# Kernel tuning notes

Measured on AMD Instinct MI355X. Metric: run time of the kernel, lower is better.

The kernel has to match this reference:

```python
import jax, jax.numpy as jnp
import numpy as np

B, S, D = 2, 2048, 2048
H, DK, DV, L = 16, 128, 128, 64


def setup_inputs() -> dict:
    key = jax.random.key(0)
    ks = jax.random.split(key, 16)
    sc = lambda fan_in: 1.0 / np.sqrt(fan_in)
    inp = {
        "queries": jax.random.normal(ks[0], (B, S, D), jnp.float32),
        "keys": jax.random.normal(ks[1], (B, S, D), jnp.float32),
        "values": jax.random.normal(ks[2], (B, S, D), jnp.float32),
        # weights stored [in, out]
        "Wq": jax.random.normal(ks[3], (D, DK * H), jnp.float32) * sc(D),
        "bq": jnp.zeros((DK * H,), jnp.float32),
        "Wlk": jax.random.normal(ks[4], (D, L * H), jnp.float32) * sc(D),
        "blk": jnp.zeros((L * H,), jnp.float32),
        "Wlv": jax.random.normal(ks[5], (D, L * H), jnp.float32) * sc(D),
        "blv": jnp.zeros((L * H,), jnp.float32),
        "Wkr": jax.random.normal(ks[6], (L, DK), jnp.float32) * sc(L),
        "bkr": jnp.zeros((DK,), jnp.float32),
        "Wvr": jax.random.normal(ks[7], (L, DV), jnp.float32) * sc(L),
        "bvr": jnp.zeros((DV,), jnp.float32),
        "Wo": jax.random.normal(ks[8], (DV * H, D), jnp.float32) * sc(DV * H),
        "bo": jnp.zeros((D,), jnp.float32),
    }
    return inp


def reference(queries, keys, values, Wq, bq, Wlk, blk, Wlv, blv, Wkr, bkr, Wvr, bvr, Wo, bo):
    b, sq, _ = queries.shape
    sk = keys.shape[1]
    # query projection -> [b, h, sq, dk]
    q = (queries @ Wq + bq).reshape(b, sq, H, DK).transpose(0, 2, 1, 3)
    # low-rank latent KV -> [b, sk, h, L]
    lat_k = (keys @ Wlk + blk).reshape(b, sk, H, L)
    lat_v = (values @ Wlv + blv).reshape(b, sk, H, L)
    # reconstruction -> [b, h, sk, dk/dv]
    k = (lat_k @ Wkr + bkr).transpose(0, 2, 1, 3)
    v = (lat_v @ Wvr + bvr).transpose(0, 2, 1, 3)
    scores = jnp.einsum("bhqd,bhkd->bhqk", q, k) / np.sqrt(DK).astype(np.float32)
    causal = jnp.triu(jnp.ones((sq, sk), dtype=bool), k=1)
    scores = jnp.where(causal, -jnp.inf, scores)
    attn = jax.nn.softmax(scores, axis=-1)
    out = jnp.einsum("bhqk,bhkd->bhqd", attn, v)
    out = out.transpose(0, 2, 1, 3).reshape(b, sq, H * DV)
    return out @ Wo + bo
```

## Files before the change

### kernel.cpp

```cpp
#include <hip/hip_runtime.h>
#include <hip/hip_bf16.h>

#define B_SZ    2
#define S_LEN   2048
#define D_MODEL 2048
#define N_HEADS 16
#define D_HEAD  128
#define L_RANK  64
#define M_ROWS  (B_SZ * S_LEN)
#define KD      2048
#define NT      (KD / 32)
#define NTK     (KD / 64)

typedef short          bf16x8 __attribute__((ext_vector_type(8)));
typedef float          f32x4  __attribute__((ext_vector_type(4)));
typedef float          f32x16 __attribute__((ext_vector_type(16)));
typedef unsigned short us4v   __attribute__((ext_vector_type(4)));
typedef unsigned short us8v   __attribute__((ext_vector_type(8)));
typedef unsigned int   u32x4  __attribute__((ext_vector_type(4)));

#define SCALE_Q 0.127517432f

static __device__ __forceinline__ unsigned short f2bf(float f) {
    unsigned int u = __float_as_uint(f);
    u += 0x7FFFu + ((u >> 16) & 1u);
    return (unsigned short)(u >> 16);
}

static __device__ __forceinline__ void gload16(const void* g, void* l) {
    __builtin_amdgcn_global_load_lds(
        (const __attribute__((address_space(1))) unsigned int*)g,
        (__attribute__((address_space(3))) unsigned int*)l, 16, 0, 0);
}

static __device__ __forceinline__ bf16x8 ds_read128(const unsigned short* p) {
    bf16x8 r;
    unsigned int a = (unsigned int)(size_t)
        (const __attribute__((address_space(3))) unsigned short*)p;
    asm volatile("ds_read_b128 %0, %1" : "=&v"(r) : "v"(a));
    return r;
}

static __device__ __forceinline__ float exp2_hw(float x) {
    float r; asm("v_exp_f32 %0, %1" : "=v"(r) : "v"(x)); return r;
}
static __device__ __forceinline__ unsigned int cvtpk_bf16(float a, float b) {
    unsigned int r; asm("v_cvt_pk_bf16_f32 %0, %1, %2" : "=v"(r) : "v"(a), "v"(b)); return r;
}

__global__ __launch_bounds__(256) void prep_kernel(
    const float* __restrict__ q_in, const float* __restrict__ k_in,
    const float* __restrict__ v_in,
    const float* __restrict__ Wq, const float* __restrict__ Wlk,
    const float* __restrict__ Wlv, const float* __restrict__ Wo,
    const float* __restrict__ Wkr, const float* __restrict__ Wvr,
    unsigned short* __restrict__ q_o, unsigned short* __restrict__ k_o,
    unsigned short* __restrict__ v_o,
    unsigned short* __restrict__ WqT, unsigned short* __restrict__ WlkT,
    unsigned short* __restrict__ WlvT, unsigned short* __restrict__ WoT,
    unsigned short* __restrict__ WkrT, unsigned short* __restrict__ WvrT)
{
    __shared__ float tl[64][69];
    const int bid = blockIdx.x, tid = threadIdx.x;

    if (bid < 12288) {
        const int z = bid >> 12;
        const float* in = z == 0 ? q_in : (z == 1 ? k_in : v_in);
        unsigned short* out = z == 0 ? q_o : (z == 1 ? k_o : v_o);
        size_t i = ((size_t)(bid & 4095) * 256 + tid) * 8;
        float4 a = *(const float4*)&in[i];
        float4 b = *(const float4*)&in[i + 4];
        us8v o = { f2bf(a.x), f2bf(a.y), f2bf(a.z), f2bf(a.w),
                   f2bf(b.x), f2bf(b.y), f2bf(b.z), f2bf(b.w) };
        *(us8v*)&out[i] = o;
    } else if (bid < 16384) {
        const int t = bid - 12288;
        const int z = t >> 10;
        const int y = (t & 1023) >> 5, x = t & 31;
        const int Nz = (z == 1 || z == 2) ? 1024 : 2048;
        if (x * 64 >= Nz) return;
        const float* W = z == 0 ? Wq : (z == 1 ? Wlk : (z == 2 ? Wlv : Wo));
        unsigned short* WT = z == 0 ? WqT : (z == 1 ? WlkT : (z == 2 ? WlvT : WoT));
        const int k0 = y * 64, n0 = x * 64;
        #pragma unroll
        for (int c = 0; c < 4; ++c) {
            int idx = c * 256 + tid;
            int r = idx >> 4, c4 = (idx & 15) * 4;
            float4 v = *(const float4*)&W[(size_t)(k0 + r) * Nz + n0 + c4];
            tl[r][c4] = v.x; tl[r][c4 + 1] = v.y; tl[r][c4 + 2] = v.z; tl[r][c4 + 3] = v.w;
        }
        __syncthreads();
        #pragma unroll
        for (int c = 0; c < 2; ++c) {
            int idx = c * 256 + tid;
            int nr = idx >> 3, s = idx & 7;
            us8v o;
            #pragma unroll
            for (int j = 0; j < 8; ++j) o[j] = f2bf(tl[s * 8 + j][nr]);
            *(us8v*)&WT[(size_t)(n0 + nr) * KD + k0 + s * 8] = o;
        }
    } else {
        #pragma unroll 1
        for (int t2 = 0; t2 < 2; ++t2) {
            const float* W = t2 ? Wvr : Wkr;
            unsigned short* WT = t2 ? WvrT : WkrT;
            for (int i = 0; i < 32; ++i) {
                int e = i * 256 + tid;
                int d = e >> 6, l = e & 63;
                WT[d * 64 + l] = f2bf(W[l * 128 + d]);
            }
        }
    }
}

__global__ __launch_bounds__(512) void stage1_8p_kernel(
    const unsigned short* __restrict__ Aq, const unsigned short* __restrict__ Ak,
    const unsigned short* __restrict__ Av,
    const unsigned short* __restrict__ WqT, const unsigned short* __restrict__ WlkT,
    const unsigned short* __restrict__ WlvT,
    const float* __restrict__ bq, const float* __restrict__ blk,
    const float* __restrict__ blv,
    unsigned short* __restrict__ q_bf, unsigned short* __restrict__ lat_k,
    unsigned short* __restrict__ lat_v)
{
    __shared__ unsigned short Al[2][2][256 * 32];
    __shared__ unsigned short Bl[2][2][256 * 32];

    const int bid = blockIdx.x;
    const int swz = (bid & 7) * 32 + (bid >> 3);
    int z, rem, row0, col0, Nz;
    if (swz < 128)      { z = 0; rem = swz;       row0 = (rem >> 3) * 256; col0 = (rem & 7) * 256; Nz = 2048; }
    else if (swz < 192) { z = 1; rem = swz - 128; row0 = (rem >> 2) * 256; col0 = (rem & 3) * 256; Nz = 1024; }
    else                { z = 2; rem = swz - 192; row0 = (rem >> 2) * 256; col0 = (rem & 3) * 256; Nz = 1024; }

    const unsigned short* A    = z == 0 ? Aq  : (z == 1 ? Ak   : Av);
    const unsigned short* Bt   = z == 0 ? WqT : (z == 1 ? WlkT : WlvT);
    const float*          bias = z == 0 ? bq  : (z == 1 ? blk  : blv);
    unsigned short*       C    = z == 0 ? q_bf : (z == 1 ? lat_k : lat_v);

    const int tid = threadIdx.x;
    const int lane = tid & 63, wid = tid >> 6;
    const int lr = lane & 15, lg = lane >> 4;
    const int wm = wid >> 2, wn = wid & 3;

    const int lin0 = tid, lin1 = 512 + tid;
    const int rS0 = lin0 >> 2, rS1 = lin1 >> 2;
    const int cS0 = (lin0 & 3) ^ ((rS0 >> 1) & 3);
    const int cS1 = (lin1 & 3) ^ ((rS1 >> 1) & 3);
    const unsigned short* aS0 = A  + (size_t)(row0 + rS0) * KD + cS0 * 8;
    const unsigned short* aS1 = A  + (size_t)(row0 + rS1) * KD + cS1 * 8;
    const unsigned short* bS0 = Bt + (size_t)(col0 + rS0) * KD + cS0 * 8;
    const unsigned short* bS1 = Bt + (size_t)(col0 + rS1) * KD + cS1 * 8;
    const int d0 = lin0 * 8, d1 = lin1 * 8;

    int aoff[8], boff[4];
    #pragma unroll
    for (int m = 0; m < 8; ++m) {
        int row = wm * 128 + m * 16 + lr;
        aoff[m] = row * 32 + ((lg ^ ((row >> 1) & 3)) * 8);
    }
    #pragma unroll
    for (int n = 0; n < 4; ++n) {
        int row = wn * 64 + n * 16 + lr;
        boff[n] = row * 32 + ((lg ^ ((row >> 1) & 3)) * 8);
    }

    f32x4 acc[8][4];
    #pragma unroll
    for (int m = 0; m < 8; ++m)
        #pragma unroll
        for (int n = 0; n < 4; ++n) acc[m][n] = (f32x4){0.f, 0.f, 0.f, 0.f};

#define STAGE_A(buf, kh, kt) do { \
        gload16(aS0 + (size_t)(kt) * 64 + (kh) * 32, &Al[buf][kh][d0]); \
        gload16(aS1 + (size_t)(kt) * 64 + (kh) * 32, &Al[buf][kh][d1]); } while (0)
#define STAGE_B(buf, kh, kt) do { \
        gload16(bS0 + (size_t)(kt) * 64 + (kh) * 32, &Bl[buf][kh][d0]); \
        gload16(bS1 + (size_t)(kt) * 64 + (kh) * 32, &Bl[buf][kh][d1]); } while (0)

    STAGE_A(0, 0, 0); STAGE_B(0, 0, 0); STAGE_A(0, 1, 0); STAGE_B(0, 1, 0);

    #pragma unroll 1
    for (int t = 0; t < NTK; ++t) {
        const int cur = t & 1, nxt = cur ^ 1;
        const bool more = (t + 1 < NTK);

        asm volatile("s_waitcnt vmcnt(4)" ::: "memory");
        __builtin_amdgcn_s_barrier();
        asm volatile("" ::: "memory");

        bf16x8 af[8], bf0, bf1;
        if (more) STAGE_A(nxt, 0, t + 1);
        #pragma unroll
        for (int m = 0; m < 8; ++m) af[m] = ds_read128(&Al[cur][0][aoff[m]]);
        bf0 = ds_read128(&Bl[cur][0][boff[0]]);
        bf1 = ds_read128(&Bl[cur][0][boff[1]]);
        asm volatile("s_waitcnt lgkmcnt(0)" ::: "memory");
        __builtin_amdgcn_sched_barrier(0);
        __builtin_amdgcn_s_setprio(1);
        #pragma unroll
        for (int m = 0; m < 8; ++m) {
            acc[m][0] = __builtin_amdgcn_mfma_f32_16x16x32_bf16(af[m], bf0, acc[m][0], 0, 0, 0);
            acc[m][1] = __builtin_amdgcn_mfma_f32_16x16x32_bf16(af[m], bf1, acc[m][1], 0, 0, 0);
        }
        __builtin_amdgcn_s_setprio(0);

        if (more) STAGE_B(nxt, 0, t + 1);
        bf0 = ds_read128(&Bl[cur][0][boff[2]]);
        bf1 = ds_read128(&Bl[cur][0][boff[3]]);
        asm volatile("s_waitcnt lgkmcnt(0)" ::: "memory");
        __builtin_amdgcn_sched_barrier(0);
        __builtin_amdgcn_s_setprio(1);
        #pragma unroll
        for (int m = 0; m < 8; ++m) {
            acc[m][2] = __builtin_amdgcn_mfma_f32_16x16x32_bf16(af[m], bf0, acc[m][2], 0, 0, 0);
            acc[m][3] = __builtin_amdgcn_mfma_f32_16x16x32_bf16(af[m], bf1, acc[m][3], 0, 0, 0);
        }
        __builtin_amdgcn_s_setprio(0);

        if (more) asm volatile("s_waitcnt vmcnt(4)" ::: "memory");
        else      asm volatile("s_waitcnt vmcnt(0)" ::: "memory");
        __builtin_amdgcn_s_barrier();
        asm volatile("" ::: "memory");

        if (more) STAGE_A(nxt, 1, t + 1);
        #pragma unroll
        for (int m = 0; m < 8; ++m) af[m] = ds_read128(&Al[cur][1][aoff[m]]);
        bf0 = ds_read128(&Bl[cur][1][boff[0]]);
        bf1 = ds_read128(&Bl[cur][1][boff[1]]);
        asm volatile("s_waitcnt lgkmcnt(0)" ::: "memory");
        __builtin_amdgcn_sched_barrier(0);
        __builtin_amdgcn_s_setprio(1);
        #pragma unroll
        for (int m = 0; m < 8; ++m) {
            acc[m][0] = __builtin_amdgcn_mfma_f32_16x16x32_bf16(af[m], bf0, acc[m][0], 0, 0, 0);
            acc[m][1] = __builtin_amdgcn_mfma_f32_16x16x32_bf16(af[m], bf1, acc[m][1], 0, 0, 0);
        }
        __builtin_amdgcn_s_setprio(0);

        if (more) STAGE_B(nxt, 1, t + 1);
        bf0 = ds_read128(&Bl[cur][1][boff[2]]);
        bf1 = ds_read128(&Bl[cur][1][boff[3]]);
        asm volatile("s_waitcnt lgkmcnt(0)" ::: "memory");
        __builtin_amdgcn_sched_barrier(0);
        __builtin_amdgcn_s_setprio(1);
        #pragma unroll
        for (int m = 0; m < 8; ++m) {
            acc[m][2] = __builtin_amdgcn_mfma_f32_16x16x32_bf16(af[m], bf0, acc[m][2], 0, 0, 0);
            acc[m][3] = __builtin_amdgcn_mfma_f32_16x16x32_bf16(af[m], bf1, acc[m][3], 0, 0, 0);
        }
        __builtin_amdgcn_s_setprio(0);
    }
#undef STAGE_A
#undef STAGE_B

    float bv[4];
    #pragma unroll
    for (int n = 0; n < 4; ++n) bv[n] = bias[col0 + wn * 64 + n * 16 + lr];
    const float omul = (z == 0) ? SCALE_Q : 1.0f;

    #pragma unroll
    for (int m = 0; m < 8; ++m) {
        #pragma unroll
        for (int n = 0; n < 4; ++n) {
            const int col = col0 + wn * 64 + n * 16 + lr;
            const int rowb = row0 + wm * 128 + m * 16 + lg * 4;
            #pragma unroll
            for (int j = 0; j < 4; ++j)
                C[(size_t)(rowb + j) * Nz + col] = f2bf((acc[m][n][j] + bv[n]) * omul);
        }
    }
}

__global__ __launch_bounds__(512) void out_gemm8p_kernel(
    const unsigned short* __restrict__ A,
    const unsigned short* __restrict__ Bt,
    const float* __restrict__ bias,
    float* __restrict__ C)
{
    __shared__ unsigned short Al[2][2][128 * 32];
    __shared__ unsigned short Bl[2][2][256 * 32];

    const int bid = blockIdx.x;
    const int swz = (bid & 7) * 32 + (bid >> 3);
    const int row0 = (swz >> 3) * 128, col0 = (swz & 7) * 256;

    const int tid = threadIdx.x;
    const int lane = tid & 63, wid = tid >> 6;
    const int lr = lane & 15, lg = lane >> 4;
    const int wm = wid >> 2, wn = wid & 3;

    const int rA = tid >> 2;
    const int cA = (tid & 3) ^ ((rA >> 1) & 3);
    const unsigned short* aS = A + (size_t)(row0 + rA) * KD + cA * 8;
    const int dA = tid * 8;
    const int lin0 = tid, lin1 = 512 + tid;
    const int rB0 = lin0 >> 2, rB1 = lin1 >> 2;
    const int cB0 = (lin0 & 3) ^ ((rB0 >> 1) & 3);
    const int cB1 = (lin1 & 3) ^ ((rB1 >> 1) & 3);
    const unsigned short* bS0 = Bt + (size_t)(col0 + rB0) * KD + cB0 * 8;
    const unsigned short* bS1 = Bt + (size_t)(col0 + rB1) * KD + cB1 * 8;
    const int dB0 = lin0 * 8, dB1 = lin1 * 8;

    int aoff[4], boff[4];
    #pragma unroll
    for (int m = 0; m < 4; ++m) {
        int row = wm * 64 + m * 16 + lr;
        aoff[m] = row * 32 + ((lg ^ ((row >> 1) & 3)) * 8);
    }
    #pragma unroll
    for (int n = 0; n < 4; ++n) {
        int row = wn * 64 + n * 16 + lr;
        boff[n] = row * 32 + ((lg ^ ((row >> 1) & 3)) * 8);
    }

    f32x4 acc[4][4];
    #pragma unroll
    for (int m = 0; m < 4; ++m)
        #pragma unroll
        for (int n = 0; n < 4; ++n) acc[m][n] = (f32x4){0.f, 0.f, 0.f, 0.f};

#define STAGE_A(buf, kh, kt) \
        gload16(aS + (size_t)(kt) * 64 + (kh) * 32, &Al[buf][kh][dA])
#define STAGE_B(buf, kh, kt) do { \
        gload16(bS0 + (size_t)(kt) * 64 + (kh) * 32, &Bl[buf][kh][dB0]); \
        gload16(bS1 + (size_t)(kt) * 64 + (kh) * 32, &Bl[buf][kh][dB1]); } while (0)

    STAGE_A(0, 0, 0); STAGE_B(0, 0, 0); STAGE_A(0, 1, 0); STAGE_B(0, 1, 0);

    #pragma unroll 1
    for (int t = 0; t < NTK; ++t) {
        const int cur = t & 1, nxt = cur ^ 1;
        const bool more = (t + 1 < NTK);

        asm volatile("s_waitcnt vmcnt(3)" ::: "memory");
        __builtin_amdgcn_s_barrier();
        asm volatile("" ::: "memory");

        bf16x8 af[4], bf0, bf1;
        if (more) STAGE_A(nxt, 0, t + 1);
        #pragma unroll
        for (int m = 0; m < 4; ++m) af[m] = ds_read128(&Al[cur][0][aoff[m]]);
        bf0 = ds_read128(&Bl[cur][0][boff[0]]);
        bf1 = ds_read128(&Bl[cur][0][boff[1]]);
        asm volatile("s_waitcnt lgkmcnt(0)" ::: "memory");
        __builtin_amdgcn_sched_barrier(0);
        __builtin_amdgcn_s_setprio(1);
        #pragma unroll
        for (int m = 0; m < 4; ++m) {
            acc[m][0] = __builtin_amdgcn_mfma_f32_16x16x32_bf16(af[m], bf0, acc[m][0], 0, 0, 0);
            acc[m][1] = __builtin_amdgcn_mfma_f32_16x16x32_bf16(af[m], bf1, acc[m][1], 0, 0, 0);
        }
        __builtin_amdgcn_s_setprio(0);

        if (more) STAGE_B(nxt, 0, t + 1);
        bf0 = ds_read128(&Bl[cur][0][boff[2]]);
        bf1 = ds_read128(&Bl[cur][0][boff[3]]);
        asm volatile("s_waitcnt lgkmcnt(0)" ::: "memory");
        __builtin_amdgcn_sched_barrier(0);
        __builtin_amdgcn_s_setprio(1);
        #pragma unroll
        for (int m = 0; m < 4; ++m) {
            acc[m][2] = __builtin_amdgcn_mfma_f32_16x16x32_bf16(af[m], bf0, acc[m][2], 0, 0, 0);
            acc[m][3] = __builtin_amdgcn_mfma_f32_16x16x32_bf16(af[m], bf1, acc[m][3], 0, 0, 0);
        }
        __builtin_amdgcn_s_setprio(0);

        if (more) asm volatile("s_waitcnt vmcnt(3)" ::: "memory");
        else      asm volatile("s_waitcnt vmcnt(0)" ::: "memory");
        __builtin_amdgcn_s_barrier();
        asm volatile("" ::: "memory");

        if (more) STAGE_A(nxt, 1, t + 1);
        #pragma unroll
        for (int m = 0; m < 4; ++m) af[m] = ds_read128(&Al[cur][1][aoff[m]]);
        bf0 = ds_read128(&Bl[cur][1][boff[0]]);
        bf1 = ds_read128(&Bl[cur][1][boff[1]]);
        asm volatile("s_waitcnt lgkmcnt(0)" ::: "memory");
        __builtin_amdgcn_sched_barrier(0);
        __builtin_amdgcn_s_setprio(1);
        #pragma unroll
        for (int m = 0; m < 4; ++m) {
            acc[m][0] = __builtin_amdgcn_mfma_f32_16x16x32_bf16(af[m], bf0, acc[m][0], 0, 0, 0);
            acc[m][1] = __builtin_amdgcn_mfma_f32_16x16x32_bf16(af[m], bf1, acc[m][1], 0, 0, 0);
        }
        __builtin_amdgcn_s_setprio(0);

        if (more) STAGE_B(nxt, 1, t + 1);
        bf0 = ds_read128(&Bl[cur][1][boff[2]]);
        bf1 = ds_read128(&Bl[cur][1][boff[3]]);
        asm volatile("s_waitcnt lgkmcnt(0)" ::: "memory");
        __builtin_amdgcn_sched_barrier(0);
        __builtin_amdgcn_s_setprio(1);
        #pragma unroll
        for (int m = 0; m < 4; ++m) {
            acc[m][2] = __builtin_amdgcn_mfma_f32_16x16x32_bf16(af[m], bf0, acc[m][2], 0, 0, 0);
            acc[m][3] = __builtin_amdgcn_mfma_f32_16x16x32_bf16(af[m], bf1, acc[m][3], 0, 0, 0);
        }
        __builtin_amdgcn_s_setprio(0);
    }
#undef STAGE_A
#undef STAGE_B

    float bv[4];
    #pragma unroll
    for (int n = 0; n < 4; ++n) bv[n] = bias[col0 + wn * 64 + n * 16 + lr];
    #pragma unroll
    for (int m = 0; m < 4; ++m)
        #pragma unroll
        for (int n = 0; n < 4; ++n) {
            const int col = col0 + wn * 64 + n * 16 + lr;
            const int rowb = row0 + wm * 64 + m * 16 + lg * 4;
            #pragma unroll
            for (int j = 0; j < 4; ++j)
                C[(size_t)(rowb + j) * D_MODEL + col] = acc[m][n][j] + bv[n];
        }
}

__global__ __launch_bounds__(256) void recon_kernel(
    const unsigned short* __restrict__ lat_k, const unsigned short* __restrict__ lat_v,
    const unsigned short* __restrict__ WkrT, const unsigned short* __restrict__ WvrT,
    const float* __restrict__ bkr, const float* __restrict__ bvr,
    unsigned short* __restrict__ k_bf, unsigned short* __restrict__ v_t)
{
    __shared__ unsigned short Alds[128 * 64];
    __shared__ unsigned short Blds[128 * 64];

    const int flat = blockIdx.x;
    const int swz = (flat & 7) * 128 + (flat >> 3);
    const int z = swz >> 9;
    const int rem = swz & 511;
    const int h = rem >> 5;
    const int r0 = (rem & 31) * 128;

    const unsigned short* lat = z ? lat_v : lat_k;
    const unsigned short* WT  = z ? WvrT : WkrT;
    const float* bias = z ? bvr : bkr;

    const int tid = threadIdx.x;
    const int lane = tid & 63, wid = tid >> 6;
    const int lr = lane & 15, lg = lane >> 4;
    const int wm = wid >> 1, wn = wid & 1;

    #pragma unroll
    for (int c = 0; c < 4; ++c) {
        int e = c * 256 + tid;
        int row = e >> 3, pc = e & 7;
        gload16(lat + (size_t)(r0 + row) * 1024 + h * 64 + ((pc ^ (row & 7)) * 8),
                Alds + e * 8);
    }
    #pragma unroll
    for (int c = 0; c < 4; ++c) {
        int e = c * 256 + tid;
        int d = e >> 3, pc = e & 7;
        gload16(WT + (size_t)d * 64 + ((pc ^ (d & 7)) * 8), Blds + e * 8);
    }
    __syncthreads();

    f32x4 acc[4][4];
    #pragma unroll
    for (int m = 0; m < 4; ++m)
        #pragma unroll
        for (int n = 0; n < 4; ++n) acc[m][n] = (f32x4){0.f, 0.f, 0.f, 0.f};

    #pragma unroll
    for (int ks = 0; ks < 2; ++ks) {
        bf16x8 af[4], bfv[4];
        #pragma unroll
        for (int m = 0; m < 4; ++m) {
            int row = wm * 64 + m * 16 + lr;
            af[m] = *(const bf16x8*)&Alds[row * 64 + (((ks * 4 + lg) ^ (row & 7)) * 8)];
        }
        #pragma unroll
        for (int n = 0; n < 4; ++n) {
            int row = wn * 64 + n * 16 + lr;
            bfv[n] = *(const bf16x8*)&Blds[row * 64 + (((ks * 4 + lg) ^ (row & 7)) * 8)];
        }
        #pragma unroll
        for (int m = 0; m < 4; ++m)
            #pragma unroll
            for (int n = 0; n < 4; ++n)
                acc[m][n] = __builtin_amdgcn_mfma_f32_16x16x32_bf16(af[m], bfv[n], acc[m][n], 0, 0, 0);
    }

    const int b = r0 >> 11;
    float bv[4];
    #pragma unroll
    for (int n = 0; n < 4; ++n) bv[n] = bias[wn * 64 + n * 16 + lr];

    #pragma unroll
    for (int m = 0; m < 4; ++m) {
        #pragma unroll
        for (int n = 0; n < 4; ++n) {
            const int d = wn * 64 + n * 16 + lr;
            const int rowb = r0 + wm * 64 + m * 16 + lg * 4;
            if (z == 0) {
                #pragma unroll
                for (int j = 0; j < 4; ++j)
                    k_bf[(size_t)(rowb + j) * D_MODEL + h * D_HEAD + d] =
                        f2bf(acc[m][n][j] + bv[n]);
            } else {
                us4v o = { f2bf(acc[m][n][0] + bv[n]), f2bf(acc[m][n][1] + bv[n]),
                           f2bf(acc[m][n][2] + bv[n]), f2bf(acc[m][n][3] + bv[n]) };
                *(us4v*)&v_t[((size_t)(b * 16 + h) * 128 + d) * 2048 + (rowb & 2047)] = o;
            }
        }
    }
}

static __device__ __forceinline__ void flash_stage(
    const unsigned short* __restrict__ kgh,
    const unsigned short* __restrict__ vtb,
    unsigned short* Kl, unsigned short* Vl, int kv0, int tid)
{
    #pragma unroll
    for (int c = 0; c < 4; ++c) {
        int idx = c * 256 + tid;
        int r = idx >> 4, ch = idx & 15;
        gload16(kgh + (size_t)(kv0 + r) * D_MODEL + ((ch ^ (r & 7)) * 8), Kl + idx * 8);
    }
    #pragma unroll
    for (int c = 0; c < 4; ++c) {
        int idx = c * 256 + tid;
        int d = idx >> 3, ch = idx & 7;
        gload16(vtb + (size_t)d * S_LEN + kv0 + ((ch ^ (d & 7)) * 8), Vl + idx * 8);
    }
}

__global__ __launch_bounds__(256, 2) void flash_kernel(
    const unsigned short* __restrict__ Q,
    const unsigned short* __restrict__ Kg,
    const unsigned short* __restrict__ Vt,
    unsigned short* __restrict__ Og)
{
    __shared__ unsigned short Klds[2][64 * 128];
    __shared__ unsigned short Vlds[2][128 * 64];

    const int tid = threadIdx.x;
    const int lane = tid & 63, wid = tid >> 6;
    const int lc = lane & 31, hi = lane >> 5;

    const int blk = blockIdx.x;
    const int jj = blk >> 5;
    const int qt = (jj < 8) ? (15 - jj) : (jj - 8);
    const int bh = blk & 31;
    const int b = bh >> 4, h = bh & 15;
    const size_t base = (size_t)b * S_LEN * D_MODEL;
    const unsigned short* kgh = Kg + base + h * D_HEAD;
    const unsigned short* vtb = Vt + (size_t)bh * D_HEAD * S_LEN;

    const int q0w = qt * 128 + wid * 32;
    const int qcol = q0w + lc;

    bf16x8 qf[8];
    #pragma unroll
    for (int dc = 0; dc < 8; ++dc)
        qf[dc] = *(const bf16x8*)&Q[base + (size_t)qcol * D_MODEL + h * D_HEAD + dc * 16 + hi * 8];

    f32x16 o_acc[4];
    #pragma unroll
    for (int dt = 0; dt < 4; ++dt)
        #pragma unroll
        for (int r = 0; r < 16; ++r) o_acc[dt][r] = 0.f;
    float m_r = -3e38f, l_r = 0.f;

    const int kxor = lc & 7;
    const int nt = 2 * qt + 2;

    int koff[16];
    #pragma unroll
    for (int dc = 0; dc < 8; ++dc) {
        koff[2 * dc]     = lc * 128 + (((dc * 2 + hi) ^ kxor) * 8);
        koff[2 * dc + 1] = (32 + lc) * 128 + (((dc * 2 + hi) ^ kxor) * 8);
    }

    flash_stage(kgh, vtb, Klds[0], Vlds[0], 0, tid);

    #pragma unroll 1
    for (int t = 0; t < nt; ++t) {
        const int bb = t & 1;
        const int kv0 = t * 64;

        asm volatile("s_waitcnt vmcnt(0)" ::: "memory");
        __builtin_amdgcn_s_barrier();
        asm volatile("" ::: "memory");

        if (t + 1 < nt)
            flash_stage(kgh, vtb, Klds[bb ^ 1], Vlds[bb ^ 1], (t + 1) * 64, tid);

        const unsigned short* Kb = Klds[bb];
        const unsigned short* Vb = Vlds[bb];

        f32x16 s0a, s0b, s1a, s1b;
        #pragma unroll
        for (int r = 0; r < 16; ++r) { s0a[r] = 0.f; s0b[r] = 0.f; s1a[r] = 0.f; s1b[r] = 0.f; }

        bf16x8 kf[8];
        #pragma unroll
        for (int i = 0; i < 8; ++i) kf[i] = ds_read128(&Kb[koff[i]]);
        asm volatile("s_waitcnt lgkmcnt(0)" ::: "memory");
        __builtin_amdgcn_sched_barrier(0);
        __builtin_amdgcn_s_setprio(1);
        #pragma unroll
        for (int dc = 0; dc < 4; ++dc) {
            s0a = __builtin_amdgcn_mfma_f32_32x32x16_bf16(kf[2 * dc],     qf[dc], s0a, 0, 0, 0);
            s1a = __builtin_amdgcn_mfma_f32_32x32x16_bf16(kf[2 * dc + 1], qf[dc], s1a, 0, 0, 0);
        }
        __builtin_amdgcn_s_setprio(0);

        #pragma unroll
        for (int i = 0; i < 8; ++i) kf[i] = ds_read128(&Kb[koff[8 + i]]);
        asm volatile("s_waitcnt lgkmcnt(0)" ::: "memory");
        __builtin_amdgcn_sched_barrier(0);
        __builtin_amdgcn_s_setprio(1);
        #pragma unroll
        for (int dc = 0; dc < 4; ++dc) {
            s0b = __builtin_amdgcn_mfma_f32_32x32x16_bf16(kf[2 * dc],     qf[dc + 4], s0b, 0, 0, 0);
            s1b = __builtin_amdgcn_mfma_f32_32x32x16_bf16(kf[2 * dc + 1], qf[dc + 4], s1b, 0, 0, 0);
        }
        __builtin_amdgcn_s_setprio(0);

        f32x16 s0 = s0a + s0b;
        f32x16 s1 = s1a + s1b;

        if (t >= nt - 2) {
            #pragma unroll
            for (int r = 0; r < 16; ++r) {
                int krow = (r & 3) + 8 * (r >> 2) + 4 * hi;
                if (kv0 + krow > qcol)      s0[r] = -3e38f;
                if (kv0 + 32 + krow > qcol) s1[r] = -3e38f;
            }
        }

        float mt[8];
        #pragma unroll
        for (int i = 0; i < 8; ++i)
            mt[i] = fmaxf(fmaxf(s0[2 * i], s0[2 * i + 1]), fmaxf(s1[2 * i], s1[2 * i + 1]));
        float mA = fmaxf(fmaxf(mt[0], mt[1]), fmaxf(mt[2], mt[3]));
        float mB = fmaxf(fmaxf(mt[4], mt[5]), fmaxf(mt[6], mt[7]));
        float sm = fmaxf(mA, mB);
        sm = fmaxf(sm, __shfl_xor(sm, 32));

        if (__any(sm > m_r + 11.5f)) {
            float mnew = fmaxf(m_r, sm);
            float alpha = exp2_hw(m_r - mnew);
            l_r *= alpha;
            m_r = mnew;
            #pragma unroll
            for (int r = 0; r < 16; ++r) {
                float av = __shfl(alpha, (r & 3) + 8 * (r >> 2) + 4 * hi);
                #pragma unroll
                for (int dt = 0; dt < 4; ++dt) o_acc[dt][r] *= av;
            }
        }

        #pragma unroll
        for (int r = 0; r < 16; ++r) {
            s0[r] = exp2_hw(s0[r] - m_r);
            s1[r] = exp2_hw(s1[r] - m_r);
        }
        float st[8];
        #pragma unroll
        for (int i = 0; i < 8; ++i)
            st[i] = (s0[2 * i] + s0[2 * i + 1]) + (s1[2 * i] + s1[2 * i + 1]);
        l_r += ((st[0] + st[1]) + (st[2] + st[3])) + ((st[4] + st[5]) + (st[6] + st[7]));

        #pragma unroll
        for (int t32 = 0; t32 < 2; ++t32) {
            const f32x16& s = t32 ? s1 : s0;
            unsigned int c0[4], c1[4];
            #pragma unroll
            for (int g = 0; g < 4; ++g) {
                c0[g] = cvtpk_bf16(s[4 * g],     s[4 * g + 1]);
                c1[g] = cvtpk_bf16(s[4 * g + 2], s[4 * g + 3]);
            }
            bf16x8 pf[2];
            #pragma unroll
            for (int kt = 0; kt < 2; ++kt) {
                unsigned int sel0 = hi ? c0[2 * kt] : c0[2 * kt + 1];
                unsigned int sel1 = hi ? c1[2 * kt] : c1[2 * kt + 1];
                unsigned int o0 = (unsigned int)__shfl_xor((int)sel0, 32);
                unsigned int o1 = (unsigned int)__shfl_xor((int)sel1, 32);
                u32x4 uu;
                uu.x = hi ? o0 : c0[2 * kt];
                uu.y = hi ? o1 : c1[2 * kt];
                uu.z = hi ? c0[2 * kt + 1] : o0;
                uu.w = hi ? c1[2 * kt + 1] : o1;
                pf[kt] = __builtin_bit_cast(bf16x8, uu);
            }
            bf16x8 vf[8];
            #pragma unroll
            for (int kt = 0; kt < 2; ++kt)
                #pragma unroll
                for (int dt = 0; dt < 4; ++dt)
                    vf[kt * 4 + dt] = ds_read128(
                        &Vb[(dt * 32 + lc) * 64 + (((t32 * 4 + kt * 2 + hi) ^ kxor) * 8)]);
            asm volatile("s_waitcnt lgkmcnt(0)" ::: "memory");
            __builtin_amdgcn_sched_barrier(0);
            __builtin_amdgcn_s_setprio(1);
            #pragma unroll
            for (int kt = 0; kt < 2; ++kt)
                #pragma unroll
                for (int dt = 0; dt < 4; ++dt)
                    o_acc[dt] = __builtin_amdgcn_mfma_f32_32x32x16_bf16(
                        pf[kt], vf[kt * 4 + dt], o_acc[dt], 0, 0, 0);
            __builtin_amdgcn_s_setprio(0);
        }
    }

    float lt = l_r + __shfl_xor(l_r, 32);
    float inv = 1.0f / lt;
    #pragma unroll
    for (int r = 0; r < 16; ++r) {
        int qrow = (r & 3) + 8 * (r >> 2) + 4 * hi;
        float iv = __shfl(inv, qrow);
        #pragma unroll
        for (int dt = 0; dt < 4; ++dt)
            Og[base + (size_t)(q0w + qrow) * D_MODEL + h * D_HEAD + dt * 32 + lc] =
                f2bf(o_acc[dt][r] * iv);
    }
}

extern "C" void kernel_launch(void* const* d_in, const int* in_sizes, int n_in,
                              void* d_out, int out_size, void* d_ws, size_t ws_size,
                              hipStream_t stream)
{
    const float* queries = (const float*)d_in[0];
    const float* keys    = (const float*)d_in[1];
    const float* values  = (const float*)d_in[2];
    const float* Wq  = (const float*)d_in[3];
    const float* bq  = (const float*)d_in[4];
    const float* Wlk = (const float*)d_in[5];
    const float* blk = (const float*)d_in[6];
    const float* Wlv = (const float*)d_in[7];
    const float* blv = (const float*)d_in[8];
    const float* Wkr = (const float*)d_in[9];
    const float* bkr = (const float*)d_in[10];
    const float* Wvr = (const float*)d_in[11];
    const float* bvr = (const float*)d_in[12];
    const float* Wo  = (const float*)d_in[13];
    const float* bo  = (const float*)d_in[14];
    float* out = (float*)d_out;

    char* ws = (char*)d_ws;
    const size_t MB = 1024 * 1024;
    unsigned short* abf_q = (unsigned short*)(ws);
    unsigned short* abf_k = (unsigned short*)(ws + 16 * MB);
    unsigned short* abf_v = (unsigned short*)(ws + 32 * MB);
    unsigned short* q_bf  = (unsigned short*)(ws + 48 * MB);
    unsigned short* k_bf  = (unsigned short*)(ws + 64 * MB);
    unsigned short* v_t   = (unsigned short*)(ws + 80 * MB);
    unsigned short* lat_k = (unsigned short*)(ws + 96 * MB);
    unsigned short* lat_v = (unsigned short*)(ws + 104 * MB);
    unsigned short* WqT   = (unsigned short*)(ws + 112 * MB);
    unsigned short* WlkT  = (unsigned short*)(ws + 120 * MB);
    unsigned short* WlvT  = (unsigned short*)(ws + 124 * MB);
    unsigned short* WkrT  = (unsigned short*)(ws + 128 * MB);
    unsigned short* WvrT  = WkrT + 128 * 64;
    unsigned short* WoT   = (unsigned short*)(ws + 129 * MB);
    unsigned short* ao    = abf_q;

    prep_kernel<<<16385, 256, 0, stream>>>(
        queries, keys, values, Wq, Wlk, Wlv, Wo, Wkr, Wvr,
        abf_q, abf_k, abf_v, WqT, WlkT, WlvT, WoT, WkrT, WvrT);

    stage1_8p_kernel<<<256, 512, 0, stream>>>(
        abf_q, abf_k, abf_v, WqT, WlkT, WlvT, bq, blk, blv,
        q_bf, lat_k, lat_v);

    recon_kernel<<<1024, 256, 0, stream>>>(
        lat_k, lat_v, WkrT, WvrT, bkr, bvr, k_bf, v_t);

    flash_kernel<<<512, 256, 0, stream>>>(q_bf, k_bf, v_t, ao);

    out_gemm8p_kernel<<<256, 512, 0, stream>>>(ao, WoT, bo, out);
}
```

Measured before the change: 231.3 us.

## Split causal flash attention over KV chunks and merge partials in a second kernel

Each query tile's KV range is split into chunks of up to 8 tiles, launching 1280 blocks instead of 512 so the long causal rows no longer dominate the tail. Each block writes unnormalized bf16 partial outputs plus per-row max and sum. A new merge kernel combines them with log-sum-exp weighting and normalizes. The cost is extra global traffic for the partials, a second launch, and an extra bf16 rounding of the partial outputs.

```diff
diff --git a/kernel.cpp b/kernel.cpp
--- a/kernel.cpp
+++ b/kernel.cpp
@@ -25,6 +25,9 @@
     unsigned int u = __float_as_uint(f);
     u += 0x7FFFu + ((u >> 16) & 1u);
     return (unsigned short)(u >> 16);
+}
+static __device__ __forceinline__ float bf2f(unsigned short u) {
+    return __uint_as_float(((unsigned int)u) << 16);
 }
 
 static __device__ __forceinline__ void gload16(const void* g, void* l) {
@@ -527,11 +530,12 @@
     }
 }
 
-__global__ __launch_bounds__(256, 2) void flash_kernel(
+__global__ __launch_bounds__(256, 2) void flash_pk_kernel(
     const unsigned short* __restrict__ Q,
     const unsigned short* __restrict__ Kg,
     const unsigned short* __restrict__ Vt,
-    unsigned short* __restrict__ Og)
+    unsigned short* __restrict__ Op,
+    float* __restrict__ mlbuf)
 {
     __shared__ unsigned short Klds[2][64 * 128];
     __shared__ unsigned short Vlds[2][128 * 64];
@@ -540,15 +544,24 @@
     const int lane = tid & 63, wid = tid >> 6;
     const int lc = lane & 31, hi = lane >> 5;
 
-    const int blk = blockIdx.x;
-    const int jj = blk >> 5;
-    const int qt = (jj < 8) ? (15 - jj) : (jj - 8);
-    const int bh = blk & 31;
+    const int flat = blockIdx.x;
+    const int bh = flat & 31;
+    const int s = flat >> 5;
+    const int g = (s < 4) ? 0 : (s < 12) ? 1 : (s < 24) ? 2 : 3;
+    const int sp = s - 2 * g * (g + 1);
+    const int qt = 4 * g + sp / (g + 1);
+    const int ck = sp % (g + 1);
+    const int slot = bh * 40 + s;
+
     const int b = bh >> 4, h = bh & 15;
     const size_t base = (size_t)b * S_LEN * D_MODEL;
     const unsigned short* kgh = Kg + base + h * D_HEAD;
     const unsigned short* vtb = Vt + (size_t)bh * D_HEAD * S_LEN;
 
+    const int nt = 2 * qt + 2;
+    const int t0 = ck * 8;
+    const int ntl = min(8, nt - t0);
+
     const int q0w = qt * 128 + wid * 32;
     const int qcol = q0w + lc;
 
@@ -565,7 +578,6 @@
     float m_r = -3e38f, l_r = 0.f;
 
     const int kxor = lc & 7;
-    const int nt = 2 * qt + 2;
 
     int koff[16];
     #pragma unroll
@@ -574,19 +586,20 @@
         koff[2 * dc + 1] = (32 + lc) * 128 + (((dc * 2 + hi) ^ kxor) * 8);
     }
 
-    flash_stage(kgh, vtb, Klds[0], Vlds[0], 0, tid);
+    flash_stage(kgh, vtb, Klds[0], Vlds[0], t0 * 64, tid);
 
     #pragma unroll 1
-    for (int t = 0; t < nt; ++t) {
-        const int bb = t & 1;
-        const int kv0 = t * 64;
+    for (int tl = 0; tl < ntl; ++tl) {
+        const int bb = tl & 1;
+        const int tg = t0 + tl;
+        const int kv0 = tg * 64;
 
         asm volatile("s_waitcnt vmcnt(0)" ::: "memory");
         __builtin_amdgcn_s_barrier();
         asm volatile("" ::: "memory");
 
-        if (t + 1 < nt)
-            flash_stage(kgh, vtb, Klds[bb ^ 1], Vlds[bb ^ 1], (t + 1) * 64, tid);
+        if (tl + 1 < ntl)
+            flash_stage(kgh, vtb, Klds[bb ^ 1], Vlds[bb ^ 1], (tg + 1) * 64, tid);
 
         const unsigned short* Kb = Klds[bb];
         const unsigned short* Vb = Vlds[bb];
@@ -623,7 +636,7 @@
         f32x16 s0 = s0a + s0b;
         f32x16 s1 = s1a + s1b;
 
-        if (t >= nt - 2) {
+        if (tg >= nt - 2) {
             #pragma unroll
             for (int r = 0; r < 16; ++r) {
                 int krow = (r & 3) + 8 * (r >> 2) + 4 * hi;
@@ -667,12 +680,12 @@
 
         #pragma unroll
         for (int t32 = 0; t32 < 2; ++t32) {
-            const f32x16& s = t32 ? s1 : s0;
+            const f32x16& sv = t32 ? s1 : s0;
             unsigned int c0[4], c1[4];
             #pragma unroll
-            for (int g = 0; g < 4; ++g) {
-                c0[g] = cvtpk_bf16(s[4 * g],     s[4 * g + 1]);
-                c1[g] = cvtpk_bf16(s[4 * g + 2], s[4 * g + 3]);
+            for (int gq = 0; gq < 4; ++gq) {
+                c0[gq] = cvtpk_bf16(sv[4 * gq],     sv[4 * gq + 1]);
+                c1[gq] = cvtpk_bf16(sv[4 * gq + 2], sv[4 * gq + 3]);
             }
             bf16x8 pf[2];
             #pragma unroll
@@ -709,15 +722,76 @@
     }
 
     float lt = l_r + __shfl_xor(l_r, 32);
-    float inv = 1.0f / lt;
+    if (hi == 0) {
+        mlbuf[((size_t)slot * 128 + wid * 32 + lc) * 2]     = m_r;
+        mlbuf[((size_t)slot * 128 + wid * 32 + lc) * 2 + 1] = lt;
+    }
     #pragma unroll
     for (int r = 0; r < 16; ++r) {
         int qrow = (r & 3) + 8 * (r >> 2) + 4 * hi;
-        float iv = __shfl(inv, qrow);
         #pragma unroll
         for (int dt = 0; dt < 4; ++dt)
-            Og[base + (size_t)(q0w + qrow) * D_MODEL + h * D_HEAD + dt * 32 + lc] =
-                f2bf(o_acc[dt][r] * iv);
+            Op[(size_t)slot * 16384 + (wid * 32 + qrow) * 128 + dt * 32 + lc] =
+                f2bf(o_acc[dt][r]);
+    }
+}
+
+__global__ __launch_bounds__(256) void merge_kernel(
+    const unsigned short* __restrict__ Op, const float* __restrict__ mlbuf,
+    unsigned short* __restrict__ ao)
+{
+    const int bid = blockIdx.x;
+    const int bh = bid & 31, qt = bid >> 5;
+    const int b = bh >> 4, h = bh & 15;
+    const int g = qt >> 2, nch = g + 1;
+    const int slot0 = bh * 40 + 2 * g * (g + 1) + (qt & 3) * nch;
+
+    const int tid = threadIdx.x;
+    const int row = tid >> 1, colh = (tid & 1) * 64;
+
+    float m_c[4], l_c[4], w[4];
+    float mstar = -3e38f;
+    #pragma unroll
+    for (int cc = 0; cc < 4; ++cc) {
+        if (cc < nch) {
+            m_c[cc] = mlbuf[((size_t)(slot0 + cc) * 128 + row) * 2];
+            l_c[cc] = mlbuf[((size_t)(slot0 + cc) * 128 + row) * 2 + 1];
+            mstar = fmaxf(mstar, m_c[cc]);
+        }
+    }
+    float lstar = 0.f;
+    #pragma unroll
+    for (int cc = 0; cc < 4; ++cc) {
+        if (cc < nch) {
+            w[cc] = exp2_hw(m_c[cc] - mstar);
+            lstar += w[cc] * l_c[cc];
+        }
+    }
+    const float inv = 1.0f / lstar;
+
+    float acc[64];
+    #pragma unroll
+    for (int j = 0; j < 64; ++j) acc[j] = 0.f;
+    #pragma unroll
+    for (int cc = 0; cc < 4; ++cc) {
+        if (cc < nch) {
+            const unsigned short* src = Op + (size_t)(slot0 + cc) * 16384 + row * 128 + colh;
+            const float wc = w[cc];
+            #pragma unroll
+            for (int v = 0; v < 8; ++v) {
+                us8v x = *(const us8v*)&src[v * 8];
+                #pragma unroll
+                for (int j = 0; j < 8; ++j) acc[v * 8 + j] += wc * bf2f(x[j]);
+            }
+        }
+    }
+    unsigned short* dst = ao + (size_t)(b * S_LEN + qt * 128 + row) * D_MODEL + h * D_HEAD + colh;
+    #pragma unroll
+    for (int v = 0; v < 8; ++v) {
+        us8v o;
+        #pragma unroll
+        for (int j = 0; j < 8; ++j) o[j] = f2bf(acc[v * 8 + j] * inv);
+        *(us8v*)&dst[v * 8] = o;
     }
 }
 
@@ -758,6 +832,8 @@
     unsigned short* WkrT  = (unsigned short*)(ws + 128 * MB);
     unsigned short* WvrT  = WkrT + 128 * 64;
     unsigned short* WoT   = (unsigned short*)(ws + 129 * MB);
+    unsigned short* Op    = (unsigned short*)(ws + 138 * MB);
+    float*          mlb   = (float*)(ws + 179 * MB);
     unsigned short* ao    = abf_q;
 
     prep_kernel<<<16385, 256, 0, stream>>>(
@@ -771,7 +847,9 @@
     recon_kernel<<<1024, 256, 0, stream>>>(
         lat_k, lat_v, WkrT, WvrT, bkr, bvr, k_bf, v_t);
 
-    flash_kernel<<<512, 256, 0, stream>>>(q_bf, k_bf, v_t, ao);
+    flash_pk_kernel<<<1280, 256, 0, stream>>>(q_bf, k_bf, v_t, Op, mlb);
+
+    merge_kernel<<<512, 256, 0, stream>>>(Op, mlb, ao);
 
     out_gemm8p_kernel<<<256, 512, 0, stream>>>(ao, WoT, bo, out);
 }
```

After: 244.6 us. 1.06x slower.
